# Kernel tuning notes

Measured on AMD Instinct MI355X. Metric: run time of the kernel, lower is better.

## Reference

```python
import jax, jax.numpy as jnp
import numpy as np

NUM_USERS = 100_000
NUM_ITEMS = 50_000
N_TOTAL = 150_100
EMBED_DIM = 64
NUM_LAYERS = 3
N_EDGES = 3_000_000
BATCH = 4096


def setup_inputs() -> dict:
    key = jax.random.key(0)
    k1, k2, k3, k4, k5, k6 = jax.random.split(key, 6)
    node_emb = jax.random.normal(k1, (N_TOTAL, EMBED_DIM), dtype=jnp.float32) * 0.1
    # COO sparse normalized adjacency (static irregular pattern)
    adj_row = jax.random.randint(k2, (N_EDGES,), 0, N_TOTAL, dtype=jnp.int32)
    adj_col = jax.random.randint(k3, (N_EDGES,), 0, N_TOTAL, dtype=jnp.int32)
    adj_val = jax.random.uniform(k4, (N_EDGES,), dtype=jnp.float32) * 0.05
    user_ids = jax.random.randint(k5, (BATCH,), 0, NUM_USERS, dtype=jnp.int32)
    item_ids = jax.random.randint(k6, (BATCH,), 0, NUM_ITEMS, dtype=jnp.int32)
    return {"node_emb": node_emb, "adj_val": adj_val, "adj_row": adj_row,
            "adj_col": adj_col, "user_ids": user_ids, "item_ids": item_ids}


def reference(node_emb, adj_val, adj_row, adj_col, user_ids, item_ids):
    # LightGCN propagation: K sparse SpMM layers, running mean over K+1 embeddings
    emb = node_emb                       # [N, D] layer-0
    acc = emb                            # running sum instead of stack+mean
    for _ in range(NUM_LAYERS):
        # SpMM: out[r] += val * emb[c]   (COO scatter-add)
        msgs = adj_val[:, None] * emb[adj_col]          # [E, D]
        emb = jax.ops.segment_sum(msgs, adj_row, num_segments=N_TOTAL)
        acc = acc + emb
    final = acc / jnp.float32(NUM_LAYERS + 1)           # mean over layers
    users = final[:NUM_USERS]
    items = final[NUM_USERS:NUM_USERS + NUM_ITEMS]
    u = users[user_ids]                                 # [B, D]
    i = items[item_ids]                                 # [B, D]
    return (u * i).sum(axis=-1)                         # [B]
```

## Files before the change

### kernel.cpp

```cpp
#include <hip/hip_runtime.h>

#define N_TOTAL    150100
#define NUM_USERS  100000
#define DIM        64
#define BSHIFT     8
#define BROWS      (1 << BSHIFT)
#define NBUK       ((N_TOTAL + BROWS - 1) / BROWS)
#define EPB        4096
#define EPT        16
#define CAP        5632
#define RSP        260
#define CONVBLKS   ((N_TOTAL * 16 + 255) / 256)

#define VSCALE     262144.0f
#define VINV       (1.0f / 262144.0f)

__device__ __forceinline__ int wave_incl_scan(int x, int lane) {
    #pragma unroll
    for (int off = 1; off < 64; off <<= 1) {
        int y = __shfl_up(x, off, 64);
        if (lane >= off) x += y;
    }
    return x;
}

__device__ __forceinline__ float ub0(unsigned w) { return (float)(w & 0xFFu); }
__device__ __forceinline__ float ub1(unsigned w) { return (float)((w >> 8) & 0xFFu); }
__device__ __forceinline__ float ub2(unsigned w) { return (float)((w >> 16) & 0xFFu); }
__device__ __forceinline__ float ub3(unsigned w) { return (float)(w >> 24); }

__device__ __forceinline__ unsigned quant_pack(float4 f, float inv) {
    int a = __float2int_rn(f.x * inv) + 128;
    int b = __float2int_rn(f.y * inv) + 128;
    int c = __float2int_rn(f.z * inv) + 128;
    int d = __float2int_rn(f.w * inv) + 128;
    a = min(max(a, 0), 255); b = min(max(b, 0), 255);
    c = min(max(c, 0), 255); d = min(max(d, 0), 255);
    return (unsigned)a | ((unsigned)b << 8) | ((unsigned)c << 16) | ((unsigned)d << 24);
}

__global__ void __launch_bounds__(256, 4) fill_buckets(
        const int* __restrict__ rows, const int* __restrict__ cols,
        const float* __restrict__ vals, int n_edges,
        int* __restrict__ gcount,
        uint2* __restrict__ epk8) {
    __shared__ unsigned      payb[EPB];
    __shared__ unsigned char rowb[EPB];
    __shared__ short         tgtb[EPB];
    __shared__ int hist[NBUK];
    __shared__ int pref[NBUK];
    __shared__ int cur[NBUK];
    __shared__ int loc[NBUK];
    __shared__ int wtot[4];
    const int tid = threadIdx.x;
    const int lane = tid & 63, wid = tid >> 6;
    const int base = blockIdx.x * EPB;
    int end = base + EPB; if (end > n_edges) end = n_edges;
    const int cnt = end - base;

    for (int i = tid; i < NBUK; i += 256) hist[i] = 0;

    unsigned pay[EPT];
    unsigned er[EPT];
    __syncthreads();

    if (cnt == EPB) {
        #pragma unroll
        for (int g = 0; g < 4; ++g) {
            const int e = base + (g * 256 + tid) * 4;
            int4   r4 = *(const int4*)(rows + e);
            int4   c4 = *(const int4*)(cols + e);
            float4 v4 = *(const float4*)(vals + e);
            int rr[4] = { r4.x, r4.y, r4.z, r4.w };
            int cc[4] = { c4.x, c4.y, c4.z, c4.w };
            float vv[4] = { v4.x, v4.y, v4.z, v4.w };
            #pragma unroll
            for (int k = 0; k < 4; ++k) {
                const int j = g * 4 + k;
                int q = (int)(vv[k] * VSCALE + 0.5f);
                if (q > 16383) q = 16383;
                pay[j] = ((unsigned)cc[k] << 14) | (unsigned)q;
                er[j]  = (unsigned)rr[k];
                atomicAdd(&hist[rr[k] >> BSHIFT], 1);
            }
        }
    } else {
        #pragma unroll
        for (int g = 0; g < 4; ++g) {
            const int e0 = base + (g * 256 + tid) * 4;
            #pragma unroll
            for (int k = 0; k < 4; ++k) {
                const int j = g * 4 + k;
                const int e = e0 + k;
                if (e < end) {
                    int r = rows[e];
                    int q = (int)(vals[e] * VSCALE + 0.5f);
                    if (q > 16383) q = 16383;
                    pay[j] = ((unsigned)cols[e] << 14) | (unsigned)q;
                    er[j]  = (unsigned)r;
                    atomicAdd(&hist[r >> BSHIFT], 1);
                } else {
                    er[j] = 0xFFFFFFFFu;
                }
            }
        }
    }
    __syncthreads();

    for (int b = tid; b < NBUK; b += 256) {
        int h = hist[b];
        loc[b] = h ? atomicAdd(&gcount[b], h) : 0;
    }
    const int t0 = tid * 3;
    int t1 = t0 + 3; if (t1 > NBUK) t1 = NBUK;
    int s = 0;
    for (int i = t0; i < t1; ++i) s += hist[i];
    int incl = wave_incl_scan(s, lane);
    if (lane == 63) wtot[wid] = incl;
    __syncthreads();
    int wofs = 0;
    for (int w = 0; w < wid; ++w) wofs += wtot[w];
    int run = incl + wofs - s;
    for (int i = t0; i < t1; ++i) {
        int h = hist[i];
        pref[i] = run;
        cur[i] = run;
        run += h;
    }
    __syncthreads();

    #pragma unroll
    for (int j = 0; j < EPT; ++j) {
        unsigned r = er[j];
        if (r != 0xFFFFFFFFu) {
            int b = (int)(r >> BSHIFT);
            int pos = atomicAdd(&cur[b], 1);
            payb[pos] = pay[j];
            rowb[pos] = (unsigned char)(r & (BROWS - 1));
            tgtb[pos] = (short)b;
        }
    }
    __syncthreads();

    for (int i = tid; i < cnt; i += 256) {
        int b = tgtb[i];
        int o = loc[b] + (i - pref[b]);
        if (o < CAP) {
            epk8[(size_t)b * CAP + o] = make_uint2(payb[i], (unsigned)rowb[i]);
        }
    }
}

__global__ void __launch_bounds__(256) sort_conv(
        uint2* __restrict__ epk8,
        const int* __restrict__ gcount,
        int* __restrict__ rs,
        const float4* __restrict__ in4,
        unsigned* __restrict__ q, float* __restrict__ sc) {
    __shared__ unsigned      buf[CAP];
    __shared__ unsigned char rbuf[CAP];
    __shared__ int hist[BROWS];
    __shared__ int curl[BROWS];
    __shared__ int wtot[4];
    const int tid = threadIdx.x;

    if (blockIdx.x >= NBUK) {
        int t = (blockIdx.x - NBUK) * 256 + tid;
        int r = t >> 4, sl = t & 15;
        if (r >= N_TOTAL) return;
        float4 f = in4[(size_t)r * 16 + sl];
        float m = fmaxf(fmaxf(fabsf(f.x), fabsf(f.y)), fmaxf(fabsf(f.z), fabsf(f.w)));
        #pragma unroll
        for (int off = 1; off < 16; off <<= 1) m = fmaxf(m, __shfl_xor(m, off, 64));
        float inv = (m > 1e-30f) ? 127.0f / m : 0.0f;
        q[(size_t)r * 16 + sl] = quant_pack(f, inv);
        if (sl == 0) sc[r] = m * (1.0f / 127.0f);
        return;
    }

    const int lane = tid & 63, wid = tid >> 6;
    const int b = blockIdx.x;
    const size_t k0 = (size_t)b * CAP;
    int cnt = gcount[b]; if (cnt > CAP) cnt = CAP;

    hist[tid] = 0;
    __syncthreads();
    for (int i = tid; i < cnt; i += 256) {
        uint2 e = epk8[k0 + i];
        buf[i]  = e.x;
        rbuf[i] = (unsigned char)e.y;
        atomicAdd(&hist[e.y & 255u], 1);
    }
    __syncthreads();
    int s = hist[tid];
    int incl = wave_incl_scan(s, lane);
    if (lane == 63) wtot[wid] = incl;
    __syncthreads();
    int wofs = 0;
    for (int w = 0; w < wid; ++w) wofs += wtot[w];
    int ex = incl + wofs - s;
    const int rbase = b << BSHIFT;
    int nrow = N_TOTAL - rbase; if (nrow > BROWS) nrow = BROWS;
    const int o0 = 2 * b * CAP;
    if (tid < nrow) rs[b * RSP + tid] = o0 + ex;
    if (tid == 0) rs[b * RSP + nrow] = o0 + cnt;
    curl[tid] = ex;
    __syncthreads();
    unsigned* out = (unsigned*)epk8;
    for (int i = tid; i < cnt; i += 256) {
        int rl = rbuf[i];
        int pos = atomicAdd(&curl[rl], 1);
        out[o0 + pos] = buf[i];
    }
}

__device__ __forceinline__ void rowsum8(const unsigned* __restrict__ qt,
                                        const float* __restrict__ sc,
                                        const int* __restrict__ rs,
                                        const unsigned* __restrict__ epk,
                                        int r, int sl, int subbase,
                                        float4& sA, float4& sB) {
    const int* rsb = rs + (r >> BSHIFT) * RSP + (r & (BROWS - 1));
    int k0 = rsb[0], k1 = rsb[1];
    sA = make_float4(0.f, 0.f, 0.f, 0.f);
    sB = make_float4(0.f, 0.f, 0.f, 0.f);
    float corr = 0.f;
    const unsigned* qrow = qt + (sl << 1);
    unsigned pr = epk[k0 + sl];
    if (sl >= k1 - k0) pr = 0u;
    float vsl = (float)(pr & 16383u) * VINV * sc[pr >> 14];
    for (int kb = k0; kb < k1; kb += 8) {
        unsigned prn = epk[kb + 8 + sl];
        corr += vsl;
        #pragma unroll
        for (int j = 0; j < 8; ++j) {
            unsigned e = (unsigned)__shfl((int)pr, subbase + j, 64);
            float vs = __shfl(vsl, subbase + j, 64);
            int c = (int)(e >> 14);
            uint2 w = *(const uint2*)(qrow + ((size_t)c << 4));
            sA.x += vs * ub0(w.x); sA.y += vs * ub1(w.x);
            sA.z += vs * ub2(w.x); sA.w += vs * ub3(w.x);
            sB.x += vs * ub0(w.y); sB.y += vs * ub1(w.y);
            sB.z += vs * ub2(w.y); sB.w += vs * ub3(w.y);
        }
        if (sl >= k1 - (kb + 8)) prn = 0u;
        vsl = (float)(prn & 16383u) * VINV * sc[prn >> 14];
        pr = prn;
    }
    corr += __shfl_xor(corr, 1, 64);
    corr += __shfl_xor(corr, 2, 64);
    corr += __shfl_xor(corr, 4, 64);
    float c128 = 128.0f * corr;
    sA.x -= c128; sA.y -= c128; sA.z -= c128; sA.w -= c128;
    sB.x -= c128; sB.y -= c128; sB.z -= c128; sB.w -= c128;
}

__global__ void spmm_q8(const unsigned* __restrict__ qt,
                        const float* __restrict__ sc,
                        const int* __restrict__ rs,
                        const unsigned* __restrict__ epk,
                        unsigned* __restrict__ qo,
                        float* __restrict__ so) {
    int t = blockIdx.x * blockDim.x + threadIdx.x;
    int r = t >> 3;
    int sl = t & 7;
    int lane = threadIdx.x & 63;
    int subbase = lane & 56;
    if (r >= N_TOTAL) return;
    float4 sA, sB;
    rowsum8(qt, sc, rs, epk, r, sl, subbase, sA, sB);
    float mA = fmaxf(fmaxf(fabsf(sA.x), fabsf(sA.y)), fmaxf(fabsf(sA.z), fabsf(sA.w)));
    float mB = fmaxf(fmaxf(fabsf(sB.x), fabsf(sB.y)), fmaxf(fabsf(sB.z), fabsf(sB.w)));
    float m = fmaxf(mA, mB);
    m = fmaxf(m, __shfl_xor(m, 1, 64));
    m = fmaxf(m, __shfl_xor(m, 2, 64));
    m = fmaxf(m, __shfl_xor(m, 4, 64));
    float inv = (m > 1e-30f) ? 127.0f / m : 0.0f;
    uint2 o = make_uint2(quant_pack(sA, inv), quant_pack(sB, inv));
    *(uint2*)(qo + (size_t)r * 16 + (sl << 1)) = o;
    if (sl == 0) so[r] = m * (1.0f / 127.0f);
}

__device__ __forceinline__ float4 dec4(unsigned w, float s) {
    return make_float4(s * (ub0(w) - 128.0f), s * (ub1(w) - 128.0f),
                       s * (ub2(w) - 128.0f), s * (ub3(w) - 128.0f));
}

__global__ void final_dot_fused(const float4* __restrict__ emb4,
                                const unsigned* __restrict__ q1,
                                const float* __restrict__ s1,
                                const unsigned* __restrict__ q2,
                                const float* __restrict__ s2,
                                const int* __restrict__ rs,
                                const unsigned* __restrict__ epk,
                                const int* __restrict__ user_ids,
                                const int* __restrict__ item_ids,
                                float* __restrict__ out, int batch) {
    int t = blockIdx.x * blockDim.x + threadIdx.x;
    int p = t >> 4;
    int h = (t >> 3) & 1;
    int sl = t & 7;
    int lane = threadIdx.x & 63;
    int subbase = lane & 56;
    if (p >= batch) return;
    int r = h ? (NUM_USERS + item_ids[p]) : user_ids[p];

    float4 lA, lB;
    rowsum8(q2, s2, rs, epk, r, sl, subbase, lA, lB);

    float4 n0 = emb4[(size_t)r * 16 + (sl << 1)];
    float4 n1 = emb4[(size_t)r * 16 + (sl << 1) + 1];
    uint2 aw = *(const uint2*)(q1 + (size_t)r * 16 + (sl << 1));
    uint2 bw = *(const uint2*)(q2 + (size_t)r * 16 + (sl << 1));
    float sa = s1[r], sb = s2[r];
    float4 a0 = dec4(aw.x, sa), a1 = dec4(aw.y, sa);
    float4 b0 = dec4(bw.x, sb), b1 = dec4(bw.y, sb);

    float f0 = n0.x + a0.x + b0.x + lA.x;
    float f1 = n0.y + a0.y + b0.y + lA.y;
    float f2 = n0.z + a0.z + b0.z + lA.z;
    float f3 = n0.w + a0.w + b0.w + lA.w;
    float f4 = n1.x + a1.x + b1.x + lB.x;
    float f5 = n1.y + a1.y + b1.y + lB.y;
    float f6 = n1.z + a1.z + b1.z + lB.z;
    float f7 = n1.w + a1.w + b1.w + lB.w;

    float s = f0 * __shfl_xor(f0, 8, 64)
            + f1 * __shfl_xor(f1, 8, 64)
            + f2 * __shfl_xor(f2, 8, 64)
            + f3 * __shfl_xor(f3, 8, 64)
            + f4 * __shfl_xor(f4, 8, 64)
            + f5 * __shfl_xor(f5, 8, 64)
            + f6 * __shfl_xor(f6, 8, 64)
            + f7 * __shfl_xor(f7, 8, 64);
    s += __shfl_xor(s, 1, 64);
    s += __shfl_xor(s, 2, 64);
    s += __shfl_xor(s, 4, 64);
    if ((t & 15) == 0) out[p] = s * (1.0f / 16.0f);
}


static inline size_t align256(size_t x) { return (x + 255) & ~(size_t)255; }

extern "C" void kernel_launch(void* const* d_in, const int* in_sizes, int n_in,
                              void* d_out, int out_size, void* d_ws, size_t ws_size,
                              hipStream_t stream) {
    const float* node_emb = (const float*)d_in[0];
    const float* adj_val  = (const float*)d_in[1];
    const int*   adj_row  = (const int*)d_in[2];
    const int*   adj_col  = (const int*)d_in[3];
    const int*   user_ids = (const int*)d_in[4];
    const int*   item_ids = (const int*)d_in[5];
    float* out = (float*)d_out;

    const int n_edges = in_sizes[1];
    const int batch   = in_sizes[4];

    const size_t qtab_bytes = (size_t)N_TOTAL * 16 * sizeof(unsigned);
    const size_t sc_bytes   = (size_t)N_TOTAL * sizeof(float);

    char* p = (char*)d_ws;
    size_t off = 0;
    unsigned* q0 = (unsigned*)(p + off); off = align256(off + qtab_bytes);
    unsigned* q1 = (unsigned*)(p + off); off = align256(off + qtab_bytes);
    unsigned* q2 = (unsigned*)(p + off); off = align256(off + qtab_bytes);
    float* s0    = (float*)(p + off);    off = align256(off + sc_bytes);
    float* s1    = (float*)(p + off);    off = align256(off + sc_bytes);
    float* s2    = (float*)(p + off);    off = align256(off + sc_bytes);
    int* gcount  = (int*)(p + off);      off = align256(off + (size_t)NBUK * sizeof(int));
    int* rs      = (int*)(p + off);      off = align256(off + (size_t)NBUK * RSP * sizeof(int));
    uint2* epk8  = (uint2*)(p + off);    off = align256(off + (size_t)NBUK * CAP * sizeof(uint2));
    (void)ws_size;

    const int nbf = (n_edges + EPB - 1) / EPB;
    const int sblocks = ((N_TOTAL * 8) + 255) / 256;

    hipMemsetAsync(gcount, 0, (size_t)NBUK * sizeof(int), stream);

    fill_buckets<<<nbf, 256, 0, stream>>>(adj_row, adj_col, adj_val, n_edges,
                                          gcount, epk8);

    sort_conv<<<NBUK + CONVBLKS, 256, 0, stream>>>(
        epk8, gcount, rs, (const float4*)node_emb, q0, s0);

    const unsigned* epk = (const unsigned*)epk8;

    spmm_q8<<<sblocks, 256, 0, stream>>>(q0, s0, rs, epk, q1, s1);
    spmm_q8<<<sblocks, 256, 0, stream>>>(q1, s1, rs, epk, q2, s2);

    {
        int threads = batch * 16;
        final_dot_fused<<<(threads + 255) / 256, 256, 0, stream>>>(
            (const float4*)node_emb, q1, s1, q2, s2, rs, epk,
            user_ids, item_ids, out, batch);
    }
}
```

Before: 258.9 us.

## Split quantized embedding tables into two 32-dim halves with separate scales

Splits each int8 quantized node table into low and high 32-column halves, each with its own per-row scale. Each SpMM layer now runs as two launches over 32-byte rows, which shrinks the gathered table to fit better in cache. The cost is reading the edge list and row offsets twice as often, plus more kernel launches. Per-half scales also change the quantization error.

```diff
diff --git a/kernel.cpp b/kernel.cpp
--- a/kernel.cpp
+++ b/kernel.cpp
@@ -156,7 +156,8 @@
         const int* __restrict__ gcount,
         int* __restrict__ rs,
         const float4* __restrict__ in4,
-        unsigned* __restrict__ q, float* __restrict__ sc) {
+        unsigned* __restrict__ qL, unsigned* __restrict__ qH,
+        float* __restrict__ scL, float* __restrict__ scH) {
     __shared__ unsigned      buf[CAP];
     __shared__ unsigned char rbuf[CAP];
     __shared__ int hist[BROWS];
@@ -170,11 +171,15 @@
         if (r >= N_TOTAL) return;
         float4 f = in4[(size_t)r * 16 + sl];
         float m = fmaxf(fmaxf(fabsf(f.x), fabsf(f.y)), fmaxf(fabsf(f.z), fabsf(f.w)));
-        #pragma unroll
-        for (int off = 1; off < 16; off <<= 1) m = fmaxf(m, __shfl_xor(m, off, 64));
+        m = fmaxf(m, __shfl_xor(m, 1, 64));
+        m = fmaxf(m, __shfl_xor(m, 2, 64));
+        m = fmaxf(m, __shfl_xor(m, 4, 64));
         float inv = (m > 1e-30f) ? 127.0f / m : 0.0f;
-        q[(size_t)r * 16 + sl] = quant_pack(f, inv);
-        if (sl == 0) sc[r] = m * (1.0f / 127.0f);
+        unsigned w = quant_pack(f, inv);
+        if (sl < 8) qL[(size_t)r * 8 + sl] = w;
+        else        qH[(size_t)r * 8 + (sl - 8)] = w;
+        if (sl == 0) scL[r] = m * (1.0f / 127.0f);
+        if (sl == 8) scH[r] = m * (1.0f / 127.0f);
         return;
     }
 
@@ -214,18 +219,17 @@
     }
 }
 
-__device__ __forceinline__ void rowsum8(const unsigned* __restrict__ qt,
-                                        const float* __restrict__ sc,
-                                        const int* __restrict__ rs,
-                                        const unsigned* __restrict__ epk,
-                                        int r, int sl, int subbase,
-                                        float4& sA, float4& sB) {
+__device__ __forceinline__ void rowsum_half(const unsigned* __restrict__ qt,
+                                            const float* __restrict__ sc,
+                                            const int* __restrict__ rs,
+                                            const unsigned* __restrict__ epk,
+                                            int r, int sl, int subbase,
+                                            float4& sA) {
     const int* rsb = rs + (r >> BSHIFT) * RSP + (r & (BROWS - 1));
     int k0 = rsb[0], k1 = rsb[1];
     sA = make_float4(0.f, 0.f, 0.f, 0.f);
-    sB = make_float4(0.f, 0.f, 0.f, 0.f);
     float corr = 0.f;
-    const unsigned* qrow = qt + (sl << 1);
+    const unsigned* qrow = qt + sl;
     unsigned pr = epk[k0 + sl];
     if (sl >= k1 - k0) pr = 0u;
     float vsl = (float)(pr & 16383u) * VINV * sc[pr >> 14];
@@ -237,11 +241,9 @@
             unsigned e = (unsigned)__shfl((int)pr, subbase + j, 64);
             float vs = __shfl(vsl, subbase + j, 64);
             int c = (int)(e >> 14);
-            uint2 w = *(const uint2*)(qrow + ((size_t)c << 4));
-            sA.x += vs * ub0(w.x); sA.y += vs * ub1(w.x);
-            sA.z += vs * ub2(w.x); sA.w += vs * ub3(w.x);
-            sB.x += vs * ub0(w.y); sB.y += vs * ub1(w.y);
-            sB.z += vs * ub2(w.y); sB.w += vs * ub3(w.y);
+            unsigned w = qrow[(size_t)c << 3];
+            sA.x += vs * ub0(w); sA.y += vs * ub1(w);
+            sA.z += vs * ub2(w); sA.w += vs * ub3(w);
         }
         if (sl >= k1 - (kb + 8)) prn = 0u;
         vsl = (float)(prn & 16383u) * VINV * sc[prn >> 14];
@@ -252,33 +254,80 @@
     corr += __shfl_xor(corr, 4, 64);
     float c128 = 128.0f * corr;
     sA.x -= c128; sA.y -= c128; sA.z -= c128; sA.w -= c128;
-    sB.x -= c128; sB.y -= c128; sB.z -= c128; sB.w -= c128;
-}
-
-__global__ void spmm_q8(const unsigned* __restrict__ qt,
-                        const float* __restrict__ sc,
-                        const int* __restrict__ rs,
-                        const unsigned* __restrict__ epk,
-                        unsigned* __restrict__ qo,
-                        float* __restrict__ so) {
+}
+
+__global__ void spmm_half(const unsigned* __restrict__ qt,
+                          const float* __restrict__ sc,
+                          const int* __restrict__ rs,
+                          const unsigned* __restrict__ epk,
+                          unsigned* __restrict__ qo,
+                          float* __restrict__ so) {
     int t = blockIdx.x * blockDim.x + threadIdx.x;
     int r = t >> 3;
     int sl = t & 7;
     int lane = threadIdx.x & 63;
     int subbase = lane & 56;
     if (r >= N_TOTAL) return;
-    float4 sA, sB;
-    rowsum8(qt, sc, rs, epk, r, sl, subbase, sA, sB);
-    float mA = fmaxf(fmaxf(fabsf(sA.x), fabsf(sA.y)), fmaxf(fabsf(sA.z), fabsf(sA.w)));
-    float mB = fmaxf(fmaxf(fabsf(sB.x), fabsf(sB.y)), fmaxf(fabsf(sB.z), fabsf(sB.w)));
-    float m = fmaxf(mA, mB);
+    float4 sA;
+    rowsum_half(qt, sc, rs, epk, r, sl, subbase, sA);
+    float m = fmaxf(fmaxf(fabsf(sA.x), fabsf(sA.y)), fmaxf(fabsf(sA.z), fabsf(sA.w)));
     m = fmaxf(m, __shfl_xor(m, 1, 64));
     m = fmaxf(m, __shfl_xor(m, 2, 64));
     m = fmaxf(m, __shfl_xor(m, 4, 64));
     float inv = (m > 1e-30f) ? 127.0f / m : 0.0f;
-    uint2 o = make_uint2(quant_pack(sA, inv), quant_pack(sB, inv));
-    *(uint2*)(qo + (size_t)r * 16 + (sl << 1)) = o;
+    qo[(size_t)r * 8 + sl] = quant_pack(sA, inv);
     if (sl == 0) so[r] = m * (1.0f / 127.0f);
+}
+
+__device__ __forceinline__ void rowsum_dual(const unsigned* __restrict__ qtL,
+                                            const float* __restrict__ scL,
+                                            const unsigned* __restrict__ qtH,
+                                            const float* __restrict__ scH,
+                                            const int* __restrict__ rs,
+                                            const unsigned* __restrict__ epk,
+                                            int r, int sl, int subbase,
+                                            float4& lo, float4& hi) {
+    const int* rsb = rs + (r >> BSHIFT) * RSP + (r & (BROWS - 1));
+    int k0 = rsb[0], k1 = rsb[1];
+    lo = make_float4(0.f, 0.f, 0.f, 0.f);
+    hi = make_float4(0.f, 0.f, 0.f, 0.f);
+    float corrL = 0.f, corrH = 0.f;
+    unsigned pr = epk[k0 + sl];
+    if (sl >= k1 - k0) pr = 0u;
+    float qv = (float)(pr & 16383u) * VINV;
+    float vL = qv * scL[pr >> 14];
+    float vH = qv * scH[pr >> 14];
+    for (int kb = k0; kb < k1; kb += 8) {
+        unsigned prn = epk[kb + 8 + sl];
+        corrL += vL; corrH += vH;
+        #pragma unroll
+        for (int j = 0; j < 8; ++j) {
+            unsigned e = (unsigned)__shfl((int)pr, subbase + j, 64);
+            float xL = __shfl(vL, subbase + j, 64);
+            float xH = __shfl(vH, subbase + j, 64);
+            int c = (int)(e >> 14);
+            unsigned wL = qtL[((size_t)c << 3) + sl];
+            unsigned wH = qtH[((size_t)c << 3) + sl];
+            lo.x += xL * ub0(wL); lo.y += xL * ub1(wL);
+            lo.z += xL * ub2(wL); lo.w += xL * ub3(wL);
+            hi.x += xH * ub0(wH); hi.y += xH * ub1(wH);
+            hi.z += xH * ub2(wH); hi.w += xH * ub3(wH);
+        }
+        if (sl >= k1 - (kb + 8)) prn = 0u;
+        qv = (float)(prn & 16383u) * VINV;
+        vL = qv * scL[prn >> 14];
+        vH = qv * scH[prn >> 14];
+        pr = prn;
+    }
+    corrL += __shfl_xor(corrL, 1, 64);
+    corrL += __shfl_xor(corrL, 2, 64);
+    corrL += __shfl_xor(corrL, 4, 64);
+    corrH += __shfl_xor(corrH, 1, 64);
+    corrH += __shfl_xor(corrH, 2, 64);
+    corrH += __shfl_xor(corrH, 4, 64);
+    float cL = 128.0f * corrL, cH = 128.0f * corrH;
+    lo.x -= cL; lo.y -= cL; lo.z -= cL; lo.w -= cL;
+    hi.x -= cH; hi.y -= cH; hi.z -= cH; hi.w -= cH;
 }
 
 __device__ __forceinline__ float4 dec4(unsigned w, float s) {
@@ -287,10 +336,14 @@
 }
 
 __global__ void final_dot_fused(const float4* __restrict__ emb4,
-                                const unsigned* __restrict__ q1,
-                                const float* __restrict__ s1,
-                                const unsigned* __restrict__ q2,
-                                const float* __restrict__ s2,
+                                const unsigned* __restrict__ q1L,
+                                const float* __restrict__ s1L,
+                                const unsigned* __restrict__ q1H,
+                                const float* __restrict__ s1H,
+                                const unsigned* __restrict__ q2L,
+                                const float* __restrict__ s2L,
+                                const unsigned* __restrict__ q2H,
+                                const float* __restrict__ s2H,
                                 const int* __restrict__ rs,
                                 const unsigned* __restrict__ epk,
                                 const int* __restrict__ user_ids,
@@ -306,15 +359,14 @@
     int r = h ? (NUM_USERS + item_ids[p]) : user_ids[p];
 
     float4 lA, lB;
-    rowsum8(q2, s2, rs, epk, r, sl, subbase, lA, lB);
-
-    float4 n0 = emb4[(size_t)r * 16 + (sl << 1)];
-    float4 n1 = emb4[(size_t)r * 16 + (sl << 1) + 1];
-    uint2 aw = *(const uint2*)(q1 + (size_t)r * 16 + (sl << 1));
-    uint2 bw = *(const uint2*)(q2 + (size_t)r * 16 + (sl << 1));
-    float sa = s1[r], sb = s2[r];
-    float4 a0 = dec4(aw.x, sa), a1 = dec4(aw.y, sa);
-    float4 b0 = dec4(bw.x, sb), b1 = dec4(bw.y, sb);
+    rowsum_dual(q2L, s2L, q2H, s2H, rs, epk, r, sl, subbase, lA, lB);
+
+    float4 n0 = emb4[(size_t)r * 16 + sl];
+    float4 n1 = emb4[(size_t)r * 16 + 8 + sl];
+    float4 a0 = dec4(q1L[(size_t)r * 8 + sl], s1L[r]);
+    float4 a1 = dec4(q1H[(size_t)r * 8 + sl], s1H[r]);
+    float4 b0 = dec4(q2L[(size_t)r * 8 + sl], s2L[r]);
+    float4 b1 = dec4(q2H[(size_t)r * 8 + sl], s2H[r]);
 
     float f0 = n0.x + a0.x + b0.x + lA.x;
     float f1 = n0.y + a0.y + b0.y + lA.y;
@@ -356,17 +408,23 @@
     const int n_edges = in_sizes[1];
     const int batch   = in_sizes[4];
 
-    const size_t qtab_bytes = (size_t)N_TOTAL * 16 * sizeof(unsigned);
+    const size_t half_bytes = (size_t)N_TOTAL * 8 * sizeof(unsigned);
     const size_t sc_bytes   = (size_t)N_TOTAL * sizeof(float);
 
     char* p = (char*)d_ws;
     size_t off = 0;
-    unsigned* q0 = (unsigned*)(p + off); off = align256(off + qtab_bytes);
-    unsigned* q1 = (unsigned*)(p + off); off = align256(off + qtab_bytes);
-    unsigned* q2 = (unsigned*)(p + off); off = align256(off + qtab_bytes);
-    float* s0    = (float*)(p + off);    off = align256(off + sc_bytes);
-    float* s1    = (float*)(p + off);    off = align256(off + sc_bytes);
-    float* s2    = (float*)(p + off);    off = align256(off + sc_bytes);
+    unsigned* q0L = (unsigned*)(p + off); off = align256(off + half_bytes);
+    unsigned* q0H = (unsigned*)(p + off); off = align256(off + half_bytes);
+    unsigned* q1L = (unsigned*)(p + off); off = align256(off + half_bytes);
+    unsigned* q1H = (unsigned*)(p + off); off = align256(off + half_bytes);
+    unsigned* q2L = (unsigned*)(p + off); off = align256(off + half_bytes);
+    unsigned* q2H = (unsigned*)(p + off); off = align256(off + half_bytes);
+    float* s0L = (float*)(p + off); off = align256(off + sc_bytes);
+    float* s0H = (float*)(p + off); off = align256(off + sc_bytes);
+    float* s1L = (float*)(p + off); off = align256(off + sc_bytes);
+    float* s1H = (float*)(p + off); off = align256(off + sc_bytes);
+    float* s2L = (float*)(p + off); off = align256(off + sc_bytes);
+    float* s2H = (float*)(p + off); off = align256(off + sc_bytes);
     int* gcount  = (int*)(p + off);      off = align256(off + (size_t)NBUK * sizeof(int));
     int* rs      = (int*)(p + off);      off = align256(off + (size_t)NBUK * RSP * sizeof(int));
     uint2* epk8  = (uint2*)(p + off);    off = align256(off + (size_t)NBUK * CAP * sizeof(uint2));
@@ -381,17 +439,19 @@
                                           gcount, epk8);
 
     sort_conv<<<NBUK + CONVBLKS, 256, 0, stream>>>(
-        epk8, gcount, rs, (const float4*)node_emb, q0, s0);
+        epk8, gcount, rs, (const float4*)node_emb, q0L, q0H, s0L, s0H);
 
     const unsigned* epk = (const unsigned*)epk8;
 
-    spmm_q8<<<sblocks, 256, 0, stream>>>(q0, s0, rs, epk, q1, s1);
-    spmm_q8<<<sblocks, 256, 0, stream>>>(q1, s1, rs, epk, q2, s2);
+    spmm_half<<<sblocks, 256, 0, stream>>>(q0L, s0L, rs, epk, q1L, s1L);
+    spmm_half<<<sblocks, 256, 0, stream>>>(q1L, s1L, rs, epk, q2L, s2L);
+    spmm_half<<<sblocks, 256, 0, stream>>>(q0H, s0H, rs, epk, q1H, s1H);
+    spmm_half<<<sblocks, 256, 0, stream>>>(q1H, s1H, rs, epk, q2H, s2H);
 
     {
         int threads = batch * 16;
         final_dot_fused<<<(threads + 255) / 256, 256, 0, stream>>>(
-            (const float4*)node_emb, q1, s1, q2, s2, rs, epk,
-            user_ids, item_ids, out, batch);
-    }
-}
+            (const float4*)node_emb, q1L, s1L, q1H, s1H, q2L, s2L, q2H, s2H,
+            rs, epk, user_ids, item_ids, out, batch);
+    }
+}
```

Measured after the change: 321.2 us. 24.1% more time.
